# Kernel tuning notes

Hardware: AMD Instinct MI355X
Metric: run time of the kernel (lower is better)

The kernel has to match this reference:

```python
import jax, jax.numpy as jnp
import numpy as np

N = 6000          # nodes
E = 192000        # edges (avg degree 32)
D = 512           # input_dim
H = 512           # hidden_dim
O = 40            # output_dim (classes)
K = 4096          # codebook_size
LAMB_EDGE = 1.0
LAMB_NODE = 1.0
COMMIT_W = 0.25
EPS = 1e-12


def _graph_conv(x, W, b, src, dst):
    """DGL GraphConv with norm='both' + ReLU activation.
    out = relu( D_in^{-1/2} A D_out^{-1/2} x W + b )"""
    ones = jnp.ones((E,), x.dtype)
    deg_out = jnp.clip(jax.ops.segment_sum(ones, src, num_segments=N), 1.0)
    deg_in = jnp.clip(jax.ops.segment_sum(ones, dst, num_segments=N), 1.0)
    xs = x * jax.lax.rsqrt(deg_out)[:, None]          # scale by src out-degree
    agg = jax.ops.segment_sum(xs[src], dst, num_segments=N)  # gather-scatter
    agg = agg * jax.lax.rsqrt(deg_in)[:, None]        # scale by dst in-degree
    return jax.nn.relu(agg @ W + b)


def _l2norm(x):
    return x * jax.lax.rsqrt(jnp.sum(x * x, axis=-1, keepdims=True) + EPS)


def setup_inputs() -> dict:
    key = jax.random.key(0)
    ks = jax.random.split(key, 13)
    s = lambda d: 1.0 / np.sqrt(d)
    return {
        "feats": jax.random.normal(ks[0], (N, D), jnp.float32),
        "W1": jax.random.normal(ks[1], (D, D), jnp.float32) * s(D),
        "b1": jnp.zeros((D,), jnp.float32),
        "W2": jax.random.normal(ks[2], (D, H), jnp.float32) * s(D),
        "b2": jnp.zeros((H,), jnp.float32),
        "Wd1": jax.random.normal(ks[3], (D, D), jnp.float32) * s(D),
        "bd1": jnp.zeros((D,), jnp.float32),
        "Wd2": jax.random.normal(ks[4], (D, D), jnp.float32) * s(D),
        "bd2": jnp.zeros((D,), jnp.float32),
        "Wl": jax.random.normal(ks[5], (H, O), jnp.float32) * s(H),
        "bl": jnp.zeros((O,), jnp.float32),
        "codebook": jax.random.normal(ks[6], (K, D), jnp.float32),
        "src": jax.random.randint(ks[7], (E,), 0, N, jnp.int32),
        "dst": jax.random.randint(ks[8], (E,), 0, N, jnp.int32),
    }


def reference(feats, W1, b1, W2, b2, Wd1, bd1, Wd2, bd2, Wl, bl, codebook, src, dst):
    # dense adjacency (as the torch module materializes via to_dense())
    adj = jnp.zeros((N, N), feats.dtype).at[dst, src].add(1.0)

    # GraphConv layer 1 (dropout is identity in eval)
    h = _graph_conv(feats, W1, b1, src, dst)           # [N, D]

    # cosine-sim VectorQuantize
    hn = _l2norm(h)
    en = _l2norm(codebook)                             # [K, D]
    dist = hn @ en.T                                   # [N, K] cosine sims
    ind = jnp.argmax(dist, axis=-1)                    # [N]
    q = en[ind]                                        # quantize with normed codebook
    commit_loss = COMMIT_W * jnp.mean((jax.lax.stop_gradient(q) - h) ** 2)
    quantized = h + jax.lax.stop_gradient(q - h)       # straight-through

    quantized_edge = quantized @ Wd1 + bd1             # decoder_1
    quantized_node = quantized @ Wd2 + bd2             # decoder_2

    feature_rec_loss = LAMB_NODE * jnp.mean((h - quantized_node) ** 2)

    adj_q = quantized_edge @ quantized_edge.T          # [N, N]
    adj_q = (adj_q - adj_q.min()) / (adj_q.max() - adj_q.min())
    edge_rec_loss = LAMB_EDGE * jnp.sqrt(jnp.mean((adj - adj_q) ** 2))

    # GraphConv layer 2 + output linear
    h2 = _graph_conv(quantized_edge, W2, b2, src, dst) # [N, H]
    out = h2 @ Wl + bl                                 # [N, O]

    loss = feature_rec_loss + edge_rec_loss + commit_loss
    return out, loss, dist
```

## Files before the change

### kernel.cpp

```cpp
#include <hip/hip_runtime.h>

typedef unsigned int u32;
typedef unsigned long long u64;

#define NN_ 6000
#define EE_ 192000
#define DD_ 512
#define KK_ 4096
#define OO_ 40
#define HSZ (1 << 19)
#define HMASK (HSZ - 1)
#define MT_A 376
#define NB_N 47

typedef __bf16 bf16x8 __attribute__((ext_vector_type(8)));
typedef float f32x4 __attribute__((ext_vector_type(4)));

__device__ __forceinline__ u32 okey(float f) {
    u32 u = __float_as_uint(f);
    return (u & 0x80000000u) ? ~u : (u | 0x80000000u);
}
__device__ __forceinline__ float dkey(u32 u) {
    u32 b = (u & 0x80000000u) ? (u ^ 0x80000000u) : ~u;
    return __uint_as_float(b);
}
__device__ __forceinline__ u64 packKey(float v, int col) {
    return ((u64)okey(v) << 32) | (u32)(~(u32)col);
}
__device__ __forceinline__ unsigned short f2bf_rne(float f) {
    u32 x = __float_as_uint(f);
    u32 r = x + 0x7fffu + ((x >> 16) & 1u);
    return (unsigned short)(r >> 16);
}
__device__ __forceinline__ void gld_lds16(void* l, const void* g) {
    __builtin_amdgcn_global_load_lds(
        (const __attribute__((address_space(1))) unsigned int*)g,
        (__attribute__((address_space(3))) unsigned int*)l, 16, 0, 0);
}
#define LGKM0 do { asm volatile("s_waitcnt lgkmcnt(0)" ::: "memory"); __builtin_amdgcn_sched_barrier(0); } while (0)

__global__ void k_deg(const int* __restrict__ src, const int* __restrict__ dst,
                      int* __restrict__ degout, int* __restrict__ degin) {
    int e = blockIdx.x * 256 + threadIdx.x;
    if (e >= EE_) return;
    atomicAdd(&degout[src[e]], 1);
    atomicAdd(&degin[dst[e]], 1);
}

__global__ void k_rsqrtdeg(const int* __restrict__ degout, const int* __restrict__ degin,
                           float* __restrict__ rout, float* __restrict__ rin) {
    int i = blockIdx.x * 256 + threadIdx.x;
    if (i >= NN_) return;
    int doV = degout[i]; if (doV < 1) doV = 1;
    int diV = degin[i];  if (diV < 1) diV = 1;
    rout[i] = rsqrtf((float)doV);
    rin[i]  = rsqrtf((float)diV);
}

__global__ void k_scan(const int* __restrict__ cnt, int* __restrict__ offs, int n) {
    __shared__ int buf[1024];
    __shared__ int carry;
    if (threadIdx.x == 0) { carry = 0; offs[0] = 0; }
    __syncthreads();
    for (int base = 0; base < n; base += 1024) {
        int i = base + threadIdx.x;
        int v = (i < n) ? cnt[i] : 0;
        buf[threadIdx.x] = v;
        __syncthreads();
        for (int off = 1; off < 1024; off <<= 1) {
            int t = (threadIdx.x >= off) ? buf[threadIdx.x - off] : 0;
            __syncthreads();
            buf[threadIdx.x] += t;
            __syncthreads();
        }
        if (i < n) offs[i + 1] = carry + buf[threadIdx.x];
        __syncthreads();
        if (threadIdx.x == 0) carry += buf[1023];
        __syncthreads();
    }
}

__global__ void k_fill(const int* __restrict__ src, const int* __restrict__ dst,
                       const int* __restrict__ offs, int* __restrict__ cursor,
                       int* __restrict__ esrc) {
    int e = blockIdx.x * 256 + threadIdx.x;
    if (e >= EE_) return;
    int d = dst[e];
    int pos = offs[d] + atomicAdd(&cursor[d], 1);
    esrc[pos] = src[e];
}

__device__ __forceinline__ void split8(const float* vals, uint4& hw, uint4& lw) {
    u32 h[4], l[4];
    #pragma unroll
    for (int j = 0; j < 4; ++j) {
        unsigned short h0 = f2bf_rne(vals[2*j]),   h1 = f2bf_rne(vals[2*j+1]);
        float hf0 = __uint_as_float((u32)h0 << 16), hf1 = __uint_as_float((u32)h1 << 16);
        unsigned short l0 = f2bf_rne(vals[2*j] - hf0), l1 = f2bf_rne(vals[2*j+1] - hf1);
        h[j] = (u32)h0 | ((u32)h1 << 16);
        l[j] = (u32)l0 | ((u32)l1 << 16);
    }
    hw = make_uint4(h[0], h[1], h[2], h[3]);
    lw = make_uint4(l[0], l[1], l[2], l[3]);
}

template<int UNW>
__global__ __launch_bounds__(256) void k_aggs(
    const float* __restrict__ X, const int* __restrict__ esrc,
    const int* __restrict__ offs, const float* __restrict__ rout,
    const float* __restrict__ rin,
    unsigned short* __restrict__ dh, unsigned short* __restrict__ dl,
    float* __restrict__ gacc) {
    __shared__ float packbuf[4][128];
    __shared__ float mred[4];
    int b = blockIdx.x;
    int xcd = b & 7;
    int slice = xcd >> 1;
    int w = threadIdx.x >> 6, lane = threadIdx.x & 63;
    int wid = ((((b >> 3) << 1) | (xcd & 1)) << 2) + w;
    const float* Xc = X + slice * 128 + lane * 2;
    float mrAcc = 0.f;
    for (int node = wid; node < NN_; node += 1024) {
        int beg = offs[node], end = offs[node + 1];
        float a0 = 0.f, a1 = 0.f, u0 = 0.f, u1 = 0.f;
        for (int e = beg; e < end; ) {
            int cnt = end - e; if (cnt > 64) cnt = 64;
            int sreg = 0; float wreg = 0.f;
            if (lane < cnt) { sreg = esrc[e + lane]; wreg = rout[sreg]; }
            int j = 0;
            for (; j + 4 <= cnt; j += 4) {
                int s0 = __shfl(sreg, j),     s1 = __shfl(sreg, j + 1);
                int s2 = __shfl(sreg, j + 2), s3 = __shfl(sreg, j + 3);
                float w0 = __shfl(wreg, j),     w1 = __shfl(wreg, j + 1);
                float w2 = __shfl(wreg, j + 2), w3 = __shfl(wreg, j + 3);
                float2 v0 = *(const float2*)(Xc + (size_t)s0 * DD_);
                float2 v1 = *(const float2*)(Xc + (size_t)s1 * DD_);
                float2 v2 = *(const float2*)(Xc + (size_t)s2 * DD_);
                float2 v3 = *(const float2*)(Xc + (size_t)s3 * DD_);
                a0 = fmaf(w0, v0.x, a0); a1 = fmaf(w0, v0.y, a1);
                a0 = fmaf(w1, v1.x, a0); a1 = fmaf(w1, v1.y, a1);
                a0 = fmaf(w2, v2.x, a0); a1 = fmaf(w2, v2.y, a1);
                a0 = fmaf(w3, v3.x, a0); a1 = fmaf(w3, v3.y, a1);
                if (UNW) {
                    u0 += (v0.x + v1.x) + (v2.x + v3.x);
                    u1 += (v0.y + v1.y) + (v2.y + v3.y);
                }
            }
            for (; j < cnt; ++j) {
                int sj = __shfl(sreg, j); float wj = __shfl(wreg, j);
                float2 v = *(const float2*)(Xc + (size_t)sj * DD_);
                a0 = fmaf(wj, v.x, a0); a1 = fmaf(wj, v.y, a1);
                if (UNW) { u0 += v.x; u1 += v.y; }
            }
            e += cnt;
        }
        float ri = rin[node];
        packbuf[w][lane * 2] = a0 * ri;
        packbuf[w][lane * 2 + 1] = a1 * ri;
        LGKM0;
        if (lane < 16) {
            uint4 hw, lw;
            split8(&packbuf[w][(lane >> 2) * 32 + (lane & 3) * 8], hw, lw);
            int kb = slice * 4 + (lane >> 2);
            int lo = (lane & 3) * 16 + (node & 15);
            size_t base = (((size_t)(node >> 4) * 16 + kb) * 64 + lo) * 8;
            *(uint4*)(dh + base) = hw;
            *(uint4*)(dl + base) = lw;
        }
        if (UNW) {
            float2 q = *(const float2*)(Xc + (size_t)node * DD_);
            mrAcc = fmaf(q.x, u0, mrAcc);
            mrAcc = fmaf(q.y, u1, mrAcc);
        }
    }
    if (UNW) {
        for (int off = 32; off; off >>= 1) mrAcc += __shfl_xor(mrAcc, off);
        if (lane == 0) mred[w] = mrAcc;
        __syncthreads();
        if (threadIdx.x == 0)
            atomicAdd(&gacc[5], mred[0] + mred[1] + mred[2] + mred[3]);
    }
}

__global__ __launch_bounds__(256) void k_cbscale(const float* __restrict__ cb,
                                                 float* __restrict__ scale, int nrows) {
    int w = threadIdx.x >> 6, lane = threadIdx.x & 63;
    for (int row = blockIdx.x * 4 + w; row < nrows; row += gridDim.x * 4) {
        const float4* p = (const float4*)(cb + (size_t)row * DD_);
        float4 x = p[lane], y = p[lane + 64];
        float s = x.x * x.x + x.y * x.y + x.z * x.z + x.w * x.w
                + y.x * y.x + y.y * y.y + y.z * y.z + y.w * y.w;
        for (int off = 32; off; off >>= 1) s += __shfl_xor(s, off);
        if (lane == 0) scale[row] = 1.0f / sqrtf(s + 1e-12f);
    }
}

__global__ __launch_bounds__(256) void k_pack(
    const float* __restrict__ src, const float* __restrict__ rowscale,
    const int* __restrict__ gidx, int nrows,
    unsigned short* __restrict__ dh, unsigned short* __restrict__ dl) {
    int u = threadIdx.x >> 6, lane = threadIdx.x & 63;
    int nmt = (nrows + 15) >> 4;
    for (int unit = blockIdx.x; unit < nmt * 4; unit += gridDim.x) {
        int mt = unit >> 2, kb = (unit & 3) * 4 + u;
        int gr = mt * 16 + (lane & 15);
        int k = kb * 32 + (lane >> 4) * 8;
        float vals[8] = {0.f,0.f,0.f,0.f,0.f,0.f,0.f,0.f};
        if (gr < nrows) {
            int row = gidx ? gidx[gr] : gr;
            float sc = rowscale ? rowscale[row] : 1.0f;
            const float4* p = (const float4*)(src + (size_t)row * DD_ + k);
            float4 a = p[0], bv = p[1];
            vals[0]=a.x*sc; vals[1]=a.y*sc; vals[2]=a.z*sc; vals[3]=a.w*sc;
            vals[4]=bv.x*sc; vals[5]=bv.y*sc; vals[6]=bv.z*sc; vals[7]=bv.w*sc;
        }
        uint4 hw, lw;
        split8(vals, hw, lw);
        size_t base = (((size_t)mt * 16 + kb) * 64 + lane) * 8;
        *(uint4*)(dh + base) = hw;
        *(uint4*)(dl + base) = lw;
    }
}

__global__ __launch_bounds__(256) void k_wpack(
    const float* __restrict__ W,
    unsigned short* __restrict__ dh, unsigned short* __restrict__ dl) {
    int u = threadIdx.x >> 6, lane = threadIdx.x & 63;
    int mt = blockIdx.x, kb = blockIdx.y * 4 + u;
    int n = mt * 16 + (lane & 15);
    int k = kb * 32 + (lane >> 4) * 8;
    float vals[8];
    #pragma unroll
    for (int j = 0; j < 8; ++j) vals[j] = W[(size_t)(k + j) * DD_ + n];
    uint4 hw, lw;
    split8(vals, hw, lw);
    size_t base = (((size_t)mt * 16 + kb) * 64 + lane) * 8;
    *(uint4*)(dh + base) = hw;
    *(uint4*)(dl + base) = lw;
}

template<int MODE, int THREE>
__global__ __launch_bounds__(256) void gemm_mfma(
    const unsigned short* __restrict__ Ah, const unsigned short* __restrict__ Al,
    const unsigned short* __restrict__ Bh, const unsigned short* __restrict__ Bl,
    float* __restrict__ Cout, const float* __restrict__ bias,
    const float* __restrict__ Ref, int relu, int Mrows,
    float* __restrict__ gacc, u32* __restrict__ minKey, u32* __restrict__ maxKey) {
    int bx, by;
    if (MODE == 1) {
        int t = blockIdx.x;
        int bi = (int)((sqrtf(8.f * (float)t + 1.f) - 1.f) * 0.5f);
        while ((bi + 1) * (bi + 2) / 2 <= t) ++bi;
        while (bi * (bi + 1) / 2 > t) --bi;
        bx = bi; by = t - bi * (bi + 1) / 2;
    } else { bx = blockIdx.x; by = blockIdx.y; }
    __shared__ char lds[32768];
    int tid = threadIdx.x;
    int wave = tid >> 6, lane = tid & 63;
    int gmtA = by * 8, gmtB = bx * 8;
    const unsigned short* garr; int gmt0;
    if (wave == 0)      { garr = Ah; gmt0 = gmtA; }
    else if (wave == 1) { garr = Al; gmt0 = gmtA; }
    else if (wave == 2) { garr = Bh; gmt0 = gmtB; }
    else                { garr = Bl; gmt0 = gmtB; }
    char* ldst = lds + wave * 8192;
    f32x4 acc[4][4];
    #pragma unroll
    for (int i = 0; i < 4; ++i)
        #pragma unroll
        for (int j = 0; j < 4; ++j) acc[i][j] = (f32x4){0.f, 0.f, 0.f, 0.f};
    int wm = wave >> 1, wn = wave & 1;
    for (int kb = 0; kb < 16; ++kb) {
        if (THREE || wave != 1) {
            #pragma unroll
            for (int t = 0; t < 8; ++t) {
                const char* g = (const char*)garr + (((size_t)(gmt0 + t) * 16 + kb) * 1024) + lane * 16;
                gld_lds16(ldst + t * 1024 + lane * 16, g);
            }
        }
        __syncthreads();
        bf16x8 a_h[4], a_l[4], b_h[4], b_l[4];
        #pragma unroll
        for (int i = 0; i < 4; ++i) {
            int at = wm * 4 + i, bt = wn * 4 + i;
            a_h[i] = *(const bf16x8*)(lds + 0     + at * 1024 + lane * 16);
            if (THREE) a_l[i] = *(const bf16x8*)(lds + 8192 + at * 1024 + lane * 16);
            b_h[i] = *(const bf16x8*)(lds + 16384 + bt * 1024 + lane * 16);
            b_l[i] = *(const bf16x8*)(lds + 24576 + bt * 1024 + lane * 16);
        }
        #pragma unroll
        for (int i = 0; i < 4; ++i)
            #pragma unroll
            for (int j = 0; j < 4; ++j) {
                acc[i][j] = __builtin_amdgcn_mfma_f32_16x16x32_bf16(a_h[i], b_h[j], acc[i][j], 0, 0, 0);
                acc[i][j] = __builtin_amdgcn_mfma_f32_16x16x32_bf16(a_h[i], b_l[j], acc[i][j], 0, 0, 0);
                if (THREE)
                    acc[i][j] = __builtin_amdgcn_mfma_f32_16x16x32_bf16(a_l[i], b_h[j], acc[i][j], 0, 0, 0);
            }
        __syncthreads();
    }
    int m_base = by * 128 + wm * 64;
    int n_base = bx * 128 + wn * 64;
    int rq = lane >> 4, cc = lane & 15;
    if (MODE == 0) {
        #pragma unroll
        for (int i = 0; i < 4; ++i) {
            int m = m_base + i * 16 + rq * 4;
            #pragma unroll
            for (int j = 0; j < 4; ++j) {
                int n = n_base + j * 16 + cc;
                #pragma unroll
                for (int r = 0; r < 4; ++r) {
                    if (m + r < NN_) Cout[(size_t)(m + r) * KK_ + n] = acc[i][j][r];
                }
            }
        }
    } else if (MODE == 2) {
        #pragma unroll
        for (int i = 0; i < 4; ++i) {
            int m = m_base + i * 16 + rq * 4;
            #pragma unroll
            for (int j = 0; j < 4; ++j) {
                int n = n_base + j * 16 + cc;
                float bv = bias[n];
                #pragma unroll
                for (int r = 0; r < 4; ++r) {
                    if (m + r < Mrows) {
                        float v = acc[i][j][r] + bv;
                        if (relu) v = fmaxf(v, 0.f);
                        Cout[(size_t)(m + r) * DD_ + n] = v;
                    }
                }
            }
        }
    } else if (MODE == 3) {
        float s = 0.f;
        #pragma unroll
        for (int i = 0; i < 4; ++i) {
            int m = m_base + i * 16 + rq * 4;
            #pragma unroll
            for (int j = 0; j < 4; ++j) {
                int n = n_base + j * 16 + cc;
                float bv = bias[n];
                #pragma unroll
                for (int r = 0; r < 4; ++r) {
                    if (m + r < Mrows) {
                        float d = Ref[(size_t)(m + r) * DD_ + n] - (acc[i][j][r] + bv);
                        s = fmaf(d, d, s);
                    }
                }
            }
        }
        float* red = (float*)lds;
        red[tid] = s; __syncthreads();
        for (int st = 128; st; st >>= 1) { if (tid < st) red[tid] += red[tid + st]; __syncthreads(); }
        if (tid == 0) atomicAdd(&gacc[3], red[0]);
    } else {
        float tsum = 0.f, tsq = 0.f, tmin = 3.4e38f, tmax = -3.4e38f;
        #pragma unroll
        for (int i = 0; i < 4; ++i) {
            #pragma unroll
            for (int j = 0; j < 4; ++j) {
                #pragma unroll
                for (int r = 0; r < 4; ++r) {
                    int m = m_base + i * 16 + rq * 4 + r;
                    int n = n_base + j * 16 + cc;
                    if (m < NN_ && n < NN_ && n >= m) {
                        float v = acc[i][j][r];
                        float w = (n > m) ? 2.f : 1.f;
                        tsum += w * v;
                        tsq  += w * v * v;
                        tmin = fminf(tmin, v);
                        tmax = fmaxf(tmax, v);
                    }
                }
            }
        }
        float* red = (float*)lds;
        red[tid] = tsum; __syncthreads();
        for (int s = 128; s; s >>= 1) { if (tid < s) red[tid] += red[tid + s]; __syncthreads(); }
        if (tid == 0) atomicAdd(&gacc[0], red[0]);
        __syncthreads();
        red[tid] = tsq; __syncthreads();
        for (int s = 128; s; s >>= 1) { if (tid < s) red[tid] += red[tid + s]; __syncthreads(); }
        if (tid == 0) atomicAdd(&gacc[1], red[0]);
        __syncthreads();
        red[tid] = tmin; __syncthreads();
        for (int s = 128; s; s >>= 1) { if (tid < s) red[tid] = fminf(red[tid], red[tid + s]); __syncthreads(); }
        if (tid == 0) atomicMin(minKey, okey(red[0]));
        __syncthreads();
        red[tid] = tmax; __syncthreads();
        for (int s = 128; s; s >>= 1) { if (tid < s) red[tid] = fmaxf(red[tid], red[tid + s]); __syncthreads(); }
        if (tid == 0) atomicMax(maxKey, okey(red[0]));
    }
}

__global__ __launch_bounds__(256) void k_rescore(
    const float* __restrict__ dist, const float* __restrict__ h,
    const float* __restrict__ rnorm, const float* __restrict__ cb,
    const float* __restrict__ scale, int* __restrict__ ind) {
    int w = threadIdx.x >> 6, lane = threadIdx.x & 63;
    for (int row = blockIdx.x * 4 + w; row < NN_; row += gridDim.x * 4) {
        const float4* dr4 = (const float4*)(dist + (size_t)row * KK_);
        float4 vbuf[16];
        float lmax = -3.4e38f;
        #pragma unroll
        for (int it = 0; it < 16; ++it) {
            float4 v = dr4[lane + it * 64];
            vbuf[it] = v;
            lmax = fmaxf(lmax, fmaxf(fmaxf(v.x, v.y), fmaxf(v.z, v.w)));
        }
        for (int off = 32; off; off >>= 1) lmax = fmaxf(lmax, __shfl_xor(lmax, off));
        float thr = lmax - 1e-3f;
        float hr = rnorm[row];
        const float* hp = h + (size_t)row * DD_;
        u64 best = 0;
        #pragma unroll 1
        for (int it = 0; it < 16; ++it) {
            float4 v = vbuf[it];
            u32 m4 = (v.x >= thr ? 1u : 0u) | (v.y >= thr ? 2u : 0u)
                   | (v.z >= thr ? 4u : 0u) | (v.w >= thr ? 8u : 0u);
            u64 bal = __ballot(m4 != 0);
            while (bal) {
                int l = __ffsll((unsigned long long)bal) - 1;
                bal &= bal - 1;
                u32 mm = __shfl(m4, l);
                while (mm) {
                    int j = __ffs(mm) - 1;
                    mm &= mm - 1;
                    int col = (l + it * 64) * 4 + j;
                    const float* cp = cb + (size_t)col * DD_;
                    float dot = 0.f;
                    #pragma unroll
                    for (int jj = 0; jj < 8; ++jj)
                        dot = fmaf(hp[lane + jj * 64], cp[lane + jj * 64], dot);
                    for (int off = 32; off; off >>= 1) dot += __shfl_xor(dot, off);
                    u64 key = packKey(dot * hr * scale[col], col);
                    if (key > best) best = key;
                }
            }
        }
        if (lane == 0) ind[row] = (int)(~(u32)(best & 0xFFFFFFFFull));
    }
}

__global__ __launch_bounds__(256) void gemm_nn(
    const float* __restrict__ A, const float* __restrict__ B,
    const float* __restrict__ bias, float* __restrict__ C,
    int M, int Ncols, int Kdim) {
    __shared__ float As[16][68];
    __shared__ float Bs[16][68];
    int tid = threadIdx.x;
    int tx = tid & 15, ty = tid >> 4;
    int m0 = blockIdx.y * 64, n0 = blockIdx.x * 64;
    float cv[4][4] = {};
    int ar = tid >> 2;
    int ak = (tid & 3) << 2;
    int am = m0 + ar;
    const float* Arow = (am < M) ? (A + (size_t)am * Kdim) : nullptr;
    int bk = tid >> 4;
    int bn = (tid & 15) << 2;
    for (int k0 = 0; k0 < Kdim; k0 += 16) {
        float4 av = make_float4(0.f, 0.f, 0.f, 0.f);
        if (Arow) av = *(const float4*)(Arow + k0 + ak);
        As[ak + 0][ar] = av.x; As[ak + 1][ar] = av.y;
        As[ak + 2][ar] = av.z; As[ak + 3][ar] = av.w;
        float4 bv = make_float4(0.f, 0.f, 0.f, 0.f);
        if (n0 + bn < Ncols)
            bv = *(const float4*)(B + (size_t)(k0 + bk) * Ncols + n0 + bn);
        Bs[bk][bn + 0] = bv.x; Bs[bk][bn + 1] = bv.y;
        Bs[bk][bn + 2] = bv.z; Bs[bk][bn + 3] = bv.w;
        __syncthreads();
        #pragma unroll
        for (int kk = 0; kk < 16; ++kk) {
            float4 a4 = *(const float4*)&As[kk][ty << 2];
            float4 b4 = *(const float4*)&Bs[kk][tx << 2];
            float ax[4] = {a4.x, a4.y, a4.z, a4.w};
            float bx[4] = {b4.x, b4.y, b4.z, b4.w};
            #pragma unroll
            for (int i = 0; i < 4; ++i)
                #pragma unroll
                for (int j = 0; j < 4; ++j)
                    cv[i][j] = fmaf(ax[i], bx[j], cv[i][j]);
        }
        __syncthreads();
    }
    #pragma unroll
    for (int i = 0; i < 4; ++i) {
        int m = m0 + (ty << 2) + i;
        if (m >= M) continue;
        #pragma unroll
        for (int j = 0; j < 4; ++j) {
            int n = n0 + (tx << 2) + j;
            if (n >= Ncols) continue;
            C[(size_t)m * Ncols + n] = cv[i][j] + bias[n];
        }
    }
}

__global__ __launch_bounds__(256) void k_losses(
    const float* __restrict__ h, const float* __restrict__ cb,
    const float* __restrict__ scale, const int* __restrict__ ind,
    float* __restrict__ gacc) {
    float s1 = 0.f;
    for (int idx = blockIdx.x * 256 + threadIdx.x; idx < NN_ * DD_; idx += gridDim.x * 256) {
        int m = idx >> 9, d = idx & 511;
        int r = ind[m];
        float q = cb[(size_t)r * DD_ + d] * scale[r];
        float dq = q - h[idx];
        s1 = fmaf(dq, dq, s1);
    }
    for (int off = 32; off; off >>= 1) s1 += __shfl_xor(s1, off);
    __shared__ float w1[4];
    int lane = threadIdx.x & 63, wv = threadIdx.x >> 6;
    if (lane == 0) w1[wv] = s1;
    __syncthreads();
    if (threadIdx.x == 0) atomicAdd(&gacc[2], w1[0] + w1[1] + w1[2] + w1[3]);
}

__global__ void k_hash(const int* __restrict__ src, const int* __restrict__ dst,
                       int* __restrict__ hkey, int* __restrict__ hcnt) {
    int e = blockIdx.x * 256 + threadIdx.x;
    if (e >= EE_) return;
    int key = dst[e] * NN_ + src[e];
    u32 h = ((u32)key * 2654435761u) & HMASK;
    while (true) {
        int old = atomicCAS(&hkey[h], -1, key);
        if (old == -1 || old == key) { atomicAdd(&hcnt[h], 1); break; }
        h = (h + 1) & HMASK;
    }
}

__global__ __launch_bounds__(256) void k_m2scan(const int* __restrict__ hcnt, float* __restrict__ gacc) {
    float s = 0.f;
    for (int i = blockIdx.x * 256 + threadIdx.x; i < HSZ; i += gridDim.x * 256) {
        float c = (float)hcnt[i];
        s = fmaf(c, c, s);
    }
    for (int off = 32; off; off >>= 1) s += __shfl_xor(s, off);
    __shared__ float w1[4];
    int lane = threadIdx.x & 63, wv = threadIdx.x >> 6;
    if (lane == 0) w1[wv] = s;
    __syncthreads();
    if (threadIdx.x == 0) atomicAdd(&gacc[4], w1[0] + w1[1] + w1[2] + w1[3]);
}

__global__ void k_final(const float* __restrict__ gacc, const u32* __restrict__ minKey,
                        const u32* __restrict__ maxKey, float* __restrict__ lossOut) {
    if (threadIdx.x != 0 || blockIdx.x != 0) return;
    double Rsum = gacc[0], Rsq = gacc[1], commitS = gacc[2], recS = gacc[3];
    double m2 = gacc[4], mr = gacc[5], ms = (double)EE_;
    double mn = (double)dkey(*minKey);
    double mx = (double)dkey(*maxKey);
    double den = mx - mn;
    double NN2 = (double)NN_ * (double)NN_;
    double sum_aq2 = (Rsq - 2.0 * mn * Rsum + NN2 * mn * mn) / (den * den);
    double sum_maq = (mr - mn * ms) / den;
    double total = sum_aq2 + m2 - 2.0 * sum_maq;
    double edge = sqrt(total / NN2);
    double commit = 0.25 * commitS / ((double)NN_ * (double)DD_);
    double rec = recS / ((double)NN_ * (double)DD_);
    *lossOut = (float)(rec + edge + commit);
}

extern "C" void kernel_launch(void* const* d_in, const int* in_sizes, int n_in,
                              void* d_out, int out_size, void* d_ws, size_t ws_size,
                              hipStream_t stream) {
    const float* feats = (const float*)d_in[0];
    const float* W1 = (const float*)d_in[1];
    const float* b1 = (const float*)d_in[2];
    const float* W2 = (const float*)d_in[3];
    const float* b2v = (const float*)d_in[4];
    const float* Wd1 = (const float*)d_in[5];
    const float* bd1 = (const float*)d_in[6];
    const float* Wd2 = (const float*)d_in[7];
    const float* bd2 = (const float*)d_in[8];
    const float* Wl = (const float*)d_in[9];
    const float* bl = (const float*)d_in[10];
    const float* cb = (const float*)d_in[11];
    const int* src = (const int*)d_in[12];
    const int* dst = (const int*)d_in[13];

    float* outF = (float*)d_out;
    float* lossOut = outF + (size_t)NN_ * OO_;
    float* distOut = lossOut + 1;

    char* w = (char*)d_ws;
    size_t off = 0;
    auto alloc = [&](size_t bytes) -> void* {
        void* p = w + off;
        off = (off + bytes + 255) & ~(size_t)255;
        return p;
    };
    float* gacc = (float*)alloc(64);
    u32* maxKey = (u32*)alloc(4);
    int* degin = (int*)alloc((size_t)NN_ * 4);
    int* degout = (int*)alloc((size_t)NN_ * 4);
    int* cursor = (int*)alloc((size_t)NN_ * 4);
    int* hcnt = (int*)alloc((size_t)HSZ * 4);
    size_t z0end = off;
    int* hkey = (int*)alloc((size_t)HSZ * 4);
    u32* minKey = (u32*)alloc(4);
    size_t z1end = off;
    int* offs = (int*)alloc((size_t)(NN_ + 1) * 4);
    int* esrc = (int*)alloc((size_t)EE_ * 4);
    float* rin = (float*)alloc((size_t)NN_ * 4);
    float* rout = (float*)alloc((size_t)NN_ * 4);
    int* ind = (int*)alloc((size_t)NN_ * 4);
    float* scale = (float*)alloc((size_t)KK_ * 4);
    float* rnorm = (float*)alloc((size_t)NN_ * 4);
    float* h = (float*)alloc((size_t)NN_ * DD_ * 4);
    float* QE = (float*)alloc((size_t)NN_ * DD_ * 4);
    const size_t NPACK = (size_t)MT_A * 16 * DD_;
    unsigned short* P1 = (unsigned short*)alloc(NPACK * 2 * 2);
    unsigned short* P2 = (unsigned short*)alloc(NPACK * 2 * 2);
    unsigned short* enp = (unsigned short*)alloc((size_t)KK_ * DD_ * 2 * 2);
    const size_t WPACK = (size_t)32 * 16 * DD_;
    unsigned short* W1p = (unsigned short*)alloc(WPACK * 2 * 2);
    unsigned short* Wd1p = (unsigned short*)alloc(WPACK * 2 * 2);
    unsigned short* Wd2p = (unsigned short*)alloc(WPACK * 2 * 2);
    unsigned short* W2p = (unsigned short*)alloc(WPACK * 2 * 2);

    unsigned short* aggp_h = P1,  *aggp_l = P1 + NPACK;
    unsigned short* qcp_h  = P1,  *qcp_l  = P1 + NPACK;
    unsigned short* ag2p_h = P1,  *ag2p_l = P1 + NPACK;
    unsigned short* hnp_h  = P2,  *hnp_l  = P2 + NPACK;
    unsigned short* QEp_h  = P2,  *QEp_l  = P2 + NPACK;
    unsigned short* enp_h  = enp, *enp_l  = enp + (size_t)KK_ * DD_;

    hipMemsetAsync(w, 0, z0end, stream);
    hipMemsetAsync(w + z0end, 0xFF, z1end - z0end, stream);

    const int TB = 256;
    k_deg<<<(EE_ + TB - 1) / TB, TB, 0, stream>>>(src, dst, degout, degin);
    k_rsqrtdeg<<<(NN_ + TB - 1) / TB, TB, 0, stream>>>(degout, degin, rout, rin);
    k_scan<<<1, 1024, 0, stream>>>(degin, offs, NN_);
    k_fill<<<(EE_ + TB - 1) / TB, TB, 0, stream>>>(src, dst, offs, cursor, esrc);
    k_wpack<<<dim3(32, 4), TB, 0, stream>>>(W1, W1p, W1p + WPACK);
    k_wpack<<<dim3(32, 4), TB, 0, stream>>>(Wd1, Wd1p, Wd1p + WPACK);
    k_wpack<<<dim3(32, 4), TB, 0, stream>>>(Wd2, Wd2p, Wd2p + WPACK);
    k_wpack<<<dim3(32, 4), TB, 0, stream>>>(W2, W2p, W2p + WPACK);
    k_aggs<0><<<1024, TB, 0, stream>>>(feats, esrc, offs, rout, rin, aggp_h, aggp_l, nullptr);
    gemm_mfma<2,1><<<dim3(4, NB_N), TB, 0, stream>>>(aggp_h, aggp_l, W1p, W1p + WPACK,
                                                     h, b1, nullptr, 1, NN_, nullptr, nullptr, nullptr);
    k_cbscale<<<256, TB, 0, stream>>>(h, rnorm, NN_);
    k_cbscale<<<256, TB, 0, stream>>>(cb, scale, KK_);
    k_pack<<<512, TB, 0, stream>>>(h, rnorm, nullptr, NN_, hnp_h, hnp_l);
    k_pack<<<512, TB, 0, stream>>>(cb, scale, nullptr, KK_, enp_h, enp_l);
    gemm_mfma<0,0><<<dim3(KK_ / 128, NB_N), TB, 0, stream>>>(hnp_h, hnp_l, enp_h, enp_l,
                                                             distOut, nullptr, nullptr, 0, NN_,
                                                             nullptr, nullptr, nullptr);
    k_rescore<<<1024, TB, 0, stream>>>(distOut, h, rnorm, cb, scale, ind);
    k_pack<<<512, TB, 0, stream>>>(cb, scale, ind, NN_, qcp_h, qcp_l);
    gemm_mfma<2,1><<<dim3(4, NB_N), TB, 0, stream>>>(qcp_h, qcp_l, Wd1p, Wd1p + WPACK,
                                                     QE, bd1, nullptr, 0, NN_, nullptr, nullptr, nullptr);
    gemm_mfma<3,1><<<dim3(4, NB_N), TB, 0, stream>>>(qcp_h, qcp_l, Wd2p, Wd2p + WPACK,
                                                     nullptr, bd2, h, 0, NN_, gacc, nullptr, nullptr);
    k_losses<<<2048, TB, 0, stream>>>(h, cb, scale, ind, gacc);
    k_pack<<<512, TB, 0, stream>>>(QE, nullptr, nullptr, NN_, QEp_h, QEp_l);
    gemm_mfma<1,1><<<NB_N * (NB_N + 1) / 2, TB, 0, stream>>>(QEp_h, QEp_l, QEp_h, QEp_l,
                                                             nullptr, nullptr, nullptr, 0, NN_,
                                                             gacc, minKey, maxKey);
    k_hash<<<(EE_ + TB - 1) / TB, TB, 0, stream>>>(src, dst, hkey, hcnt);
    k_m2scan<<<512, TB, 0, stream>>>(hcnt, gacc);
    k_aggs<1><<<1024, TB, 0, stream>>>(QE, esrc, offs, rout, rin, ag2p_h, ag2p_l, gacc);
    gemm_mfma<2,1><<<dim3(4, NB_N), TB, 0, stream>>>(ag2p_h, ag2p_l, W2p, W2p + WPACK,
                                                     h, b2v, nullptr, 1, NN_, nullptr, nullptr, nullptr);
    gemm_nn<<<dim3(1, 94), TB, 0, stream>>>(h, Wl, bl, outF, NN_, OO_, DD_);
    k_final<<<1, 64, 0, stream>>>(gacc, minKey, maxKey, lossOut);
}
```

Before: 710.8 us.

## Fuse decoder GEMMs and commit loss into one MFMA launch, use wave-shuffle reductions

```diff
diff --git a/kernel.cpp b/kernel.cpp
--- a/kernel.cpp
+++ b/kernel.cpp
@@ -12,6 +12,7 @@
 #define HMASK (HSZ - 1)
 #define MT_A 376
 #define NB_N 47
+#define WPACKE (32 * 16 * 512)
 
 typedef __bf16 bf16x8 __attribute__((ext_vector_type(8)));
 typedef float f32x4 __attribute__((ext_vector_type(4)));
@@ -245,7 +246,8 @@
     const unsigned short* __restrict__ Bh, const unsigned short* __restrict__ Bl,
     float* __restrict__ Cout, const float* __restrict__ bias,
     const float* __restrict__ Ref, int relu, int Mrows,
-    float* __restrict__ gacc, u32* __restrict__ minKey, u32* __restrict__ maxKey) {
+    float* __restrict__ gacc, u32* __restrict__ minKey, u32* __restrict__ maxKey,
+    const float* __restrict__ bias2) {
     int bx, by;
     if (MODE == 1) {
         int t = blockIdx.x;
@@ -254,21 +256,25 @@
         while (bi * (bi + 1) / 2 > t) --bi;
         bx = bi; by = t - bi * (bi + 1) / 2;
     } else { bx = blockIdx.x; by = blockIdx.y; }
+    int side = (MODE == 4) ? (bx >> 2) : 0;
+    int bxe  = (MODE == 4) ? (bx & 3) : bx;
     __shared__ char lds[32768];
+    __shared__ float wred0[4], wred1[4], wred2[4], wred3[4];
     int tid = threadIdx.x;
     int wave = tid >> 6, lane = tid & 63;
-    int gmtA = by * 8, gmtB = bx * 8;
+    int gmtA = by * 8, gmtB = bxe * 8;
     const unsigned short* garr; int gmt0;
     if (wave == 0)      { garr = Ah; gmt0 = gmtA; }
     else if (wave == 1) { garr = Al; gmt0 = gmtA; }
-    else if (wave == 2) { garr = Bh; gmt0 = gmtB; }
-    else                { garr = Bl; gmt0 = gmtB; }
+    else if (wave == 2) { garr = Bh + (size_t)side * 2 * WPACKE; gmt0 = gmtB; }
+    else                { garr = Bl + (size_t)side * 2 * WPACKE; gmt0 = gmtB; }
     char* ldst = lds + wave * 8192;
     f32x4 acc[4][4];
     #pragma unroll
     for (int i = 0; i < 4; ++i)
         #pragma unroll
         for (int j = 0; j < 4; ++j) acc[i][j] = (f32x4){0.f, 0.f, 0.f, 0.f};
+    float commitAcc = 0.f;
     int wm = wave >> 1, wn = wave & 1;
     for (int kb = 0; kb < 16; ++kb) {
         if (THREE || wave != 1) {
@@ -279,6 +285,28 @@
             }
         }
         __syncthreads();
+        if (MODE == 4 && bx == 4) {
+            int rg = tid >> 1, half = tid & 1;
+            int m = by * 128 + rg;
+            if (m < Mrows) {
+                int tt = rg >> 4, r = rg & 15;
+                const float* hp = Ref + (size_t)m * DD_ + kb * 32 + half * 16;
+                float4 h0 = ((const float4*)hp)[0], h1 = ((const float4*)hp)[1];
+                float4 h2 = ((const float4*)hp)[2], h3 = ((const float4*)hp)[3];
+                float hv[16] = {h0.x,h0.y,h0.z,h0.w, h1.x,h1.y,h1.z,h1.w,
+                                h2.x,h2.y,h2.z,h2.w, h3.x,h3.y,h3.z,h3.w};
+                #pragma unroll
+                for (int j2 = 0; j2 < 16; ++j2) {
+                    int sub = half * 2 + (j2 >> 3), j = j2 & 7;
+                    int off = tt * 1024 + (sub * 16 + r) * 16 + j * 2;
+                    u32 hb = *(const unsigned short*)(lds + off);
+                    u32 lb = *(const unsigned short*)(lds + 8192 + off);
+                    float q = __uint_as_float(hb << 16) + __uint_as_float(lb << 16);
+                    float d = q - hv[j2];
+                    commitAcc = fmaf(d, d, commitAcc);
+                }
+            }
+        }
         bf16x8 a_h[4], a_l[4], b_h[4], b_l[4];
         #pragma unroll
         for (int i = 0; i < 4; ++i) {
@@ -300,7 +328,7 @@
         __syncthreads();
     }
     int m_base = by * 128 + wm * 64;
-    int n_base = bx * 128 + wn * 64;
+    int n_base = bxe * 128 + wn * 64;
     int rq = lane >> 4, cc = lane & 15;
     if (MODE == 0) {
         #pragma unroll
@@ -315,7 +343,7 @@
                 }
             }
         }
-    } else if (MODE == 2) {
+    } else if (MODE == 2 || (MODE == 4 && side == 0)) {
         #pragma unroll
         for (int i = 0; i < 4; ++i) {
             int m = m_base + i * 16 + rq * 4;
@@ -333,7 +361,8 @@
                 }
             }
         }
-    } else if (MODE == 3) {
+    } else if (MODE == 3 || (MODE == 4 && side == 1)) {
+        const float* bs = (MODE == 4) ? bias2 : bias;
         float s = 0.f;
         #pragma unroll
         for (int i = 0; i < 4; ++i) {
@@ -341,7 +370,7 @@
             #pragma unroll
             for (int j = 0; j < 4; ++j) {
                 int n = n_base + j * 16 + cc;
-                float bv = bias[n];
+                float bv = bs[n];
                 #pragma unroll
                 for (int r = 0; r < 4; ++r) {
                     if (m + r < Mrows) {
@@ -351,10 +380,19 @@
                 }
             }
         }
-        float* red = (float*)lds;
-        red[tid] = s; __syncthreads();
-        for (int st = 128; st; st >>= 1) { if (tid < st) red[tid] += red[tid + st]; __syncthreads(); }
-        if (tid == 0) atomicAdd(&gacc[3], red[0]);
+        for (int off = 32; off; off >>= 1) s += __shfl_xor(s, off);
+        if (lane == 0) wred0[wave] = s;
+        if (MODE == 4 && bx == 4) {
+            float c = commitAcc;
+            for (int off = 32; off; off >>= 1) c += __shfl_xor(c, off);
+            if (lane == 0) wred1[wave] = c;
+        }
+        __syncthreads();
+        if (tid == 0) {
+            atomicAdd(&gacc[3], wred0[0] + wred0[1] + wred0[2] + wred0[3]);
+            if (MODE == 4 && bx == 4)
+                atomicAdd(&gacc[2], wred1[0] + wred1[1] + wred1[2] + wred1[3]);
+        }
     } else {
         float tsum = 0.f, tsq = 0.f, tmin = 3.4e38f, tmax = -3.4e38f;
         #pragma unroll
@@ -376,22 +414,20 @@
                 }
             }
         }
-        float* red = (float*)lds;
-        red[tid] = tsum; __syncthreads();
-        for (int s = 128; s; s >>= 1) { if (tid < s) red[tid] += red[tid + s]; __syncthreads(); }
-        if (tid == 0) atomicAdd(&gacc[0], red[0]);
-        __syncthreads();
-        red[tid] = tsq; __syncthreads();
-        for (int s = 128; s; s >>= 1) { if (tid < s) red[tid] += red[tid + s]; __syncthreads(); }
-        if (tid == 0) atomicAdd(&gacc[1], red[0]);
-        __syncthreads();
-        red[tid] = tmin; __syncthreads();
-        for (int s = 128; s; s >>= 1) { if (tid < s) red[tid] = fminf(red[tid], red[tid + s]); __syncthreads(); }
-        if (tid == 0) atomicMin(minKey, okey(red[0]));
-        __syncthreads();
-        red[tid] = tmax; __syncthreads();
-        for (int s = 128; s; s >>= 1) { if (tid < s) red[tid] = fmaxf(red[tid], red[tid + s]); __syncthreads(); }
-        if (tid == 0) atomicMax(maxKey, okey(red[0]));
+        for (int off = 32; off; off >>= 1) {
+            tsum += __shfl_xor(tsum, off);
+            tsq  += __shfl_xor(tsq, off);
+            tmin = fminf(tmin, __shfl_xor(tmin, off));
+            tmax = fmaxf(tmax, __shfl_xor(tmax, off));
+        }
+        if (lane == 0) { wred0[wave] = tsum; wred1[wave] = tsq; wred2[wave] = tmin; wred3[wave] = tmax; }
+        __syncthreads();
+        if (tid == 0) {
+            atomicAdd(&gacc[0], wred0[0] + wred0[1] + wred0[2] + wred0[3]);
+            atomicAdd(&gacc[1], wred1[0] + wred1[1] + wred1[2] + wred1[3]);
+            atomicMin(minKey, okey(fminf(fminf(wred2[0], wred2[1]), fminf(wred2[2], wred2[3]))));
+            atomicMax(maxKey, okey(fmaxf(fmaxf(wred3[0], wred3[1]), fmaxf(wred3[2], wred3[3]))));
+        }
     }
 }
 
@@ -496,26 +532,6 @@
             C[(size_t)m * Ncols + n] = cv[i][j] + bias[n];
         }
     }
-}
-
-__global__ __launch_bounds__(256) void k_losses(
-    const float* __restrict__ h, const float* __restrict__ cb,
-    const float* __restrict__ scale, const int* __restrict__ ind,
-    float* __restrict__ gacc) {
-    float s1 = 0.f;
-    for (int idx = blockIdx.x * 256 + threadIdx.x; idx < NN_ * DD_; idx += gridDim.x * 256) {
-        int m = idx >> 9, d = idx & 511;
-        int r = ind[m];
-        float q = cb[(size_t)r * DD_ + d] * scale[r];
-        float dq = q - h[idx];
-        s1 = fmaf(dq, dq, s1);
-    }
-    for (int off = 32; off; off >>= 1) s1 += __shfl_xor(s1, off);
-    __shared__ float w1[4];
-    int lane = threadIdx.x & 63, wv = threadIdx.x >> 6;
-    if (lane == 0) w1[wv] = s1;
-    __syncthreads();
-    if (threadIdx.x == 0) atomicAdd(&gacc[2], w1[0] + w1[1] + w1[2] + w1[3]);
 }
 
 __global__ void k_hash(const int* __restrict__ src, const int* __restrict__ dst,
@@ -642,30 +658,27 @@
     k_wpack<<<dim3(32, 4), TB, 0, stream>>>(W2, W2p, W2p + WPACK);
     k_aggs<0><<<1024, TB, 0, stream>>>(feats, esrc, offs, rout, rin, aggp_h, aggp_l, nullptr);
     gemm_mfma<2,1><<<dim3(4, NB_N), TB, 0, stream>>>(aggp_h, aggp_l, W1p, W1p + WPACK,
-                                                     h, b1, nullptr, 1, NN_, nullptr, nullptr, nullptr);
+                                                     h, b1, nullptr, 1, NN_, nullptr, nullptr, nullptr, nullptr);
     k_cbscale<<<256, TB, 0, stream>>>(h, rnorm, NN_);
     k_cbscale<<<256, TB, 0, stream>>>(cb, scale, KK_);
     k_pack<<<512, TB, 0, stream>>>(h, rnorm, nullptr, NN_, hnp_h, hnp_l);
     k_pack<<<512, TB, 0, stream>>>(cb, scale, nullptr, KK_, enp_h, enp_l);
     gemm_mfma<0,0><<<dim3(KK_ / 128, NB_N), TB, 0, stream>>>(hnp_h, hnp_l, enp_h, enp_l,
                                                              distOut, nullptr, nullptr, 0, NN_,
-                                                             nullptr, nullptr, nullptr);
+                                                             nullptr, nullptr, nullptr, nullptr);
     k_rescore<<<1024, TB, 0, stream>>>(distOut, h, rnorm, cb, scale, ind);
     k_pack<<<512, TB, 0, stream>>>(cb, scale, ind, NN_, qcp_h, qcp_l);
-    gemm_mfma<2,1><<<dim3(4, NB_N), TB, 0, stream>>>(qcp_h, qcp_l, Wd1p, Wd1p + WPACK,
-                                                     QE, bd1, nullptr, 0, NN_, nullptr, nullptr, nullptr);
-    gemm_mfma<3,1><<<dim3(4, NB_N), TB, 0, stream>>>(qcp_h, qcp_l, Wd2p, Wd2p + WPACK,
-                                                     nullptr, bd2, h, 0, NN_, gacc, nullptr, nullptr);
-    k_losses<<<2048, TB, 0, stream>>>(h, cb, scale, ind, gacc);
+    gemm_mfma<4,1><<<dim3(8, NB_N), TB, 0, stream>>>(qcp_h, qcp_l, Wd1p, Wd1p + WPACK,
+                                                     QE, bd1, h, 0, NN_, gacc, nullptr, nullptr, bd2);
     k_pack<<<512, TB, 0, stream>>>(QE, nullptr, nullptr, NN_, QEp_h, QEp_l);
     gemm_mfma<1,1><<<NB_N * (NB_N + 1) / 2, TB, 0, stream>>>(QEp_h, QEp_l, QEp_h, QEp_l,
                                                              nullptr, nullptr, nullptr, 0, NN_,
-                                                             gacc, minKey, maxKey);
+                                                             gacc, minKey, maxKey, nullptr);
     k_hash<<<(EE_ + TB - 1) / TB, TB, 0, stream>>>(src, dst, hkey, hcnt);
     k_m2scan<<<512, TB, 0, stream>>>(hcnt, gacc);
     k_aggs<1><<<1024, TB, 0, stream>>>(QE, esrc, offs, rout, rin, ag2p_h, ag2p_l, gacc);
     gemm_mfma<2,1><<<dim3(4, NB_N), TB, 0, stream>>>(ag2p_h, ag2p_l, W2p, W2p + WPACK,
-                                                     h, b2v, nullptr, 1, NN_, nullptr, nullptr, nullptr);
+                                                     h, b2v, nullptr, 1, NN_, nullptr, nullptr, nullptr, nullptr);
     gemm_nn<<<dim3(1, 94), TB, 0, stream>>>(h, Wl, bl, outF, NN_, OO_, DD_);
     k_final<<<1, 64, 0, stream>>>(gacc, minKey, maxKey, lossOut);
 }
```

Result: faster. 681.0 us (-4.2%).
